# Kernel tuning notes

Measured on AMD Instinct MI355X. Metric: run time of the kernel, lower is better.

Reference implementation:

```python
import jax, jax.numpy as jnp
import numpy as np

N_NODES = 101001  # n_user + n_item + n_attr + 1
EMBED = 64
N_EDGES = 2020020  # ~avg degree 20
EPS = 1e-12


def setup_inputs() -> dict:
    key = jax.random.key(0)
    ks = jax.random.split(key, 8)
    h0 = jax.random.normal(ks[0], (N_NODES, EMBED), dtype=jnp.float32)
    h_att = jax.random.normal(ks[1], (N_NODES, EMBED), dtype=jnp.float32)
    t_att = jax.random.normal(ks[2], (N_NODES, EMBED), dtype=jnp.float32)
    w1 = jax.random.normal(ks[3], (EMBED, EMBED), dtype=jnp.float32) * (1.0 / np.sqrt(EMBED))
    b1 = jnp.zeros((EMBED,), dtype=jnp.float32)
    w2 = jax.random.normal(ks[4], (EMBED, EMBED), dtype=jnp.float32) * (1.0 / np.sqrt(EMBED))
    b2 = jnp.zeros((EMBED,), dtype=jnp.float32)
    edge_row = jnp.sort(jax.random.randint(ks[5], (N_EDGES,), 0, N_NODES, dtype=jnp.int32))
    edge_col = jax.random.randint(ks[6], (N_EDGES,), 0, N_NODES, dtype=jnp.int32)
    return {"h0": h0, "h_att": h_att, "t_att": t_att, "w1": w1, "b1": b1,
            "w2": w2, "b2": b2, "edge_row": edge_row, "edge_col": edge_col}


def _edge_softmax(h_att, t_att, edge_row, edge_col, n):
    # per-source-node softmax over ragged neighbor lists (kg_pair)
    logits = jnp.sum(h_att[edge_row] * t_att[edge_col], axis=-1)  # [E]
    m = jax.ops.segment_max(logits, edge_row, num_segments=n)
    e = jnp.exp(logits - m[edge_row])
    s = jax.ops.segment_sum(e, edge_row, num_segments=n)
    return e / jnp.maximum(s[edge_row], EPS)  # [E]


def reference(h0, h_att, t_att, w1, b1, w2, b2, edge_row, edge_col):
    n, d = h0.shape
    w = _edge_softmax(h_att, t_att, edge_row, edge_col, n)  # sparse attention weights
    h = h0
    all_embedding = [h0]
    for (W, b) in ((w1, b1), (w2, b2)):  # k = 1, 2 of ProP_n_Layer
        # n_embedding = SpMM(sp_weight, h)
        msg = jax.ops.segment_sum(w[:, None] * h[edge_col], edge_row, num_segments=n)
        add = h + msg
        h = jax.nn.relu(add @ W.T + b)
        norm = h / jnp.maximum(jnp.linalg.norm(h, axis=-1, keepdims=True), EPS)
        all_embedding.append(norm)
        h = norm  # normalized embedding feeds the next propagation layer
    return jnp.stack(all_embedding, axis=0)  # [n_layer, N, D]
```

## Files before the change

### kernel.cpp

```cpp
#include <hip/hip_runtime.h>
#include <math.h>

#define EMBED 64

__device__ __forceinline__ float dot4(float4 a, float4 b) {
    return fmaf(a.x, b.x, fmaf(a.y, b.y, fmaf(a.z, b.z, a.w * b.w)));
}

__device__ __forceinline__ float red16(float d) {
    d += __shfl_xor(d, 1);
    d += __shfl_xor(d, 2);
    d += __shfl_xor(d, 4);
    d += __shfl_xor(d, 8);
    return d;
}

__global__ void __launch_bounds__(256, 8) rowptr_logits_kernel(
        const float* __restrict__ ha, const float* __restrict__ ta,
        const int* __restrict__ row, const int* __restrict__ col,
        int* __restrict__ rp, float* __restrict__ logits,
        int E, int N, int totalThreads, int totalWaves) {
    int tid = blockIdx.x * blockDim.x + threadIdx.x;

    for (int i = tid; i < E; i += totalThreads) {
        if (i == 0) {
            int r0 = row[0];
            for (int r = 0; r <= r0; ++r) rp[r] = 0;
        } else {
            int a = row[i - 1], b = row[i];
            for (int r = a + 1; r <= b; ++r) rp[r] = i;
        }
        if (i == E - 1) {
            int rl = row[E - 1];
            for (int r = rl + 1; r <= N; ++r) rp[r] = E;
        }
    }

    int wid = tid >> 6;
    int lane = threadIdx.x & 63;
    int eg = lane >> 4, q = lane & 15;
    const float4* ha4 = (const float4*)ha;
    const float4* ta4 = (const float4*)ta;

    for (int base = wid * 16; base < E; base += totalWaves * 16) {
        int j0 = base + eg, j1 = base + 4 + eg, j2 = base + 8 + eg, j3 = base + 12 + eg;
        int i0 = min(j0, E - 1), i1 = min(j1, E - 1);
        int i2 = min(j2, E - 1), i3 = min(j3, E - 1);
        int r0 = row[i0], r1 = row[i1], r2 = row[i2], r3 = row[i3];
        int c0 = col[i0], c1 = col[i1], c2 = col[i2], c3 = col[i3];
        float4 t0 = ta4[(size_t)c0 * 16 + q];
        float4 t1 = ta4[(size_t)c1 * 16 + q];
        float4 t2 = ta4[(size_t)c2 * 16 + q];
        float4 t3 = ta4[(size_t)c3 * 16 + q];
        float4 a0 = ha4[(size_t)r0 * 16 + q];
        float4 a1 = ha4[(size_t)r1 * 16 + q];
        float4 a2 = ha4[(size_t)r2 * 16 + q];
        float4 a3 = ha4[(size_t)r3 * 16 + q];
        float d0 = red16(dot4(a0, t0));
        float d1 = red16(dot4(a1, t1));
        float d2 = red16(dot4(a2, t2));
        float d3 = red16(dot4(a3, t3));
        if (q == 0) {
            if (j0 < E) logits[j0] = d0;
            if (j1 < E) logits[j1] = d1;
            if (j2 < E) logits[j2] = d2;
            if (j3 < E) logits[j3] = d3;
        }
    }
}

__global__ void __launch_bounds__(256) copy_softmax_kernel(
        const float* __restrict__ h0, float* __restrict__ out0, int n4,
        const int* __restrict__ rp, float* __restrict__ lw, int N,
        int totalThreads, int totalWaves) {
    int tid = blockIdx.x * blockDim.x + threadIdx.x;
    for (int i = tid; i < n4; i += totalThreads)
        ((float4*)out0)[i] = ((const float4*)h0)[i];

    int wid = tid >> 6;
    int lane = threadIdx.x & 63;
    for (int n = wid; n < N; n += totalWaves) {
        int s = rp[n], t = rp[n + 1];
        int deg = t - s;
        if (deg <= 0) continue;
        if (deg <= 64) {
            float v = (lane < deg) ? lw[s + lane] : -1e30f;
            float m = v;
            #pragma unroll
            for (int off = 32; off > 0; off >>= 1) m = fmaxf(m, __shfl_xor(m, off));
            float e = (lane < deg) ? __expf(v - m) : 0.f;
            float sum = e;
            #pragma unroll
            for (int off = 32; off > 0; off >>= 1) sum += __shfl_xor(sum, off);
            float inv = 1.f / fmaxf(sum, 1e-12f);
            if (lane < deg) lw[s + lane] = e * inv;
        } else {
            float m = -1e30f;
            for (int e = s + lane; e < t; e += 64) m = fmaxf(m, lw[e]);
            #pragma unroll
            for (int off = 32; off > 0; off >>= 1) m = fmaxf(m, __shfl_xor(m, off));
            float sum = 0.f;
            for (int e = s + lane; e < t; e += 64) sum += __expf(lw[e] - m);
            #pragma unroll
            for (int off = 32; off > 0; off >>= 1) sum += __shfl_xor(sum, off);
            float inv = 1.f / fmaxf(sum, 1e-12f);
            for (int e = s + lane; e < t; e += 64) lw[e] = __expf(lw[e] - m) * inv;
        }
    }
}

__global__ void __launch_bounds__(256, 4) prop_layer_kernel(
        const float* __restrict__ h_in,
        const float* __restrict__ W, const float* __restrict__ b,
        const int* __restrict__ col, const float* __restrict__ ew,
        const int* __restrict__ rp,
        float* __restrict__ out, int N, int totalWaves) {
    __shared__ float4 rbuf[4][17];
    int wid = (blockIdx.x * blockDim.x + threadIdx.x) >> 6;
    int lane = threadIdx.x & 63;
    int ws = threadIdx.x >> 6;
    int eg = lane >> 4, q = lane & 15;
    const float4* h4 = (const float4*)h_in;

    float4 Wr[16];
    const float4* W4 = (const float4*)W;
    #pragma unroll
    for (int p = 0; p < 16; ++p) Wr[p] = W4[lane * 16 + p];
    float bias = b[lane];

    for (int n = wid; n < N; n += totalWaves) {
        int s = rp[n], t = rp[n + 1];
        float4 self = h4[(size_t)n * 16 + q];
        float4 a0 = make_float4(0.f, 0.f, 0.f, 0.f);
        float4 a1 = make_float4(0.f, 0.f, 0.f, 0.f);
        int e0 = s;
        for (; e0 + 16 <= t; e0 += 16) {
            int i0 = e0 + eg, i1 = e0 + 4 + eg, i2 = e0 + 8 + eg, i3 = e0 + 12 + eg;
            int c0 = col[i0], c1 = col[i1], c2 = col[i2], c3 = col[i3];
            float w0 = ew[i0], w1 = ew[i1], w2 = ew[i2], w3 = ew[i3];
            float4 v0 = h4[(size_t)c0 * 16 + q];
            float4 v1 = h4[(size_t)c1 * 16 + q];
            float4 v2 = h4[(size_t)c2 * 16 + q];
            float4 v3 = h4[(size_t)c3 * 16 + q];
            a0.x = fmaf(w0, v0.x, a0.x); a0.y = fmaf(w0, v0.y, a0.y);
            a0.z = fmaf(w0, v0.z, a0.z); a0.w = fmaf(w0, v0.w, a0.w);
            a1.x = fmaf(w1, v1.x, a1.x); a1.y = fmaf(w1, v1.y, a1.y);
            a1.z = fmaf(w1, v1.z, a1.z); a1.w = fmaf(w1, v1.w, a1.w);
            a0.x = fmaf(w2, v2.x, a0.x); a0.y = fmaf(w2, v2.y, a0.y);
            a0.z = fmaf(w2, v2.z, a0.z); a0.w = fmaf(w2, v2.w, a0.w);
            a1.x = fmaf(w3, v3.x, a1.x); a1.y = fmaf(w3, v3.y, a1.y);
            a1.z = fmaf(w3, v3.z, a1.z); a1.w = fmaf(w3, v3.w, a1.w);
        }
        if (e0 < t) {
            int j0 = e0 + eg, j1 = e0 + 4 + eg, j2 = e0 + 8 + eg, j3 = e0 + 12 + eg;
            int i0 = min(j0, t - 1), i1 = min(j1, t - 1);
            int i2 = min(j2, t - 1), i3 = min(j3, t - 1);
            int c0 = col[i0], c1 = col[i1], c2 = col[i2], c3 = col[i3];
            float w0 = (j0 < t) ? ew[i0] : 0.f;
            float w1 = (j1 < t) ? ew[i1] : 0.f;
            float w2 = (j2 < t) ? ew[i2] : 0.f;
            float w3 = (j3 < t) ? ew[i3] : 0.f;
            float4 v0 = h4[(size_t)c0 * 16 + q];
            float4 v1 = h4[(size_t)c1 * 16 + q];
            float4 v2 = h4[(size_t)c2 * 16 + q];
            float4 v3 = h4[(size_t)c3 * 16 + q];
            a0.x = fmaf(w0, v0.x, a0.x); a0.y = fmaf(w0, v0.y, a0.y);
            a0.z = fmaf(w0, v0.z, a0.z); a0.w = fmaf(w0, v0.w, a0.w);
            a1.x = fmaf(w1, v1.x, a1.x); a1.y = fmaf(w1, v1.y, a1.y);
            a1.z = fmaf(w1, v1.z, a1.z); a1.w = fmaf(w1, v1.w, a1.w);
            a0.x = fmaf(w2, v2.x, a0.x); a0.y = fmaf(w2, v2.y, a0.y);
            a0.z = fmaf(w2, v2.z, a0.z); a0.w = fmaf(w2, v2.w, a0.w);
            a1.x = fmaf(w3, v3.x, a1.x); a1.y = fmaf(w3, v3.y, a1.y);
            a1.z = fmaf(w3, v3.z, a1.z); a1.w = fmaf(w3, v3.w, a1.w);
        }
        a0.x += a1.x; a0.y += a1.y; a0.z += a1.z; a0.w += a1.w;
        a0.x += __shfl_xor(a0.x, 16); a0.y += __shfl_xor(a0.y, 16);
        a0.z += __shfl_xor(a0.z, 16); a0.w += __shfl_xor(a0.w, 16);
        a0.x += __shfl_xor(a0.x, 32); a0.y += __shfl_xor(a0.y, 32);
        a0.z += __shfl_xor(a0.z, 32); a0.w += __shfl_xor(a0.w, 32);

        if (eg == 0) {
            float4 r;
            r.x = self.x + a0.x; r.y = self.y + a0.y;
            r.z = self.z + a0.z; r.w = self.w + a0.w;
            rbuf[ws][q] = r;
        }
        asm volatile("s_waitcnt lgkmcnt(0)" ::: "memory");

        float x0 = bias, x1 = 0.f, x2 = 0.f, x3 = 0.f;
        #pragma unroll
        for (int j = 0; j < 4; ++j) {
            float4 b0 = rbuf[ws][4 * j + 0];
            float4 b1 = rbuf[ws][4 * j + 1];
            float4 b2 = rbuf[ws][4 * j + 2];
            float4 b3 = rbuf[ws][4 * j + 3];
            float4 w0 = Wr[4 * j + 0], w1 = Wr[4 * j + 1];
            float4 w2 = Wr[4 * j + 2], w3 = Wr[4 * j + 3];
            x0 = fmaf(b0.x, w0.x, x0); x0 = fmaf(b0.y, w0.y, x0);
            x0 = fmaf(b0.z, w0.z, x0); x0 = fmaf(b0.w, w0.w, x0);
            x1 = fmaf(b1.x, w1.x, x1); x1 = fmaf(b1.y, w1.y, x1);
            x1 = fmaf(b1.z, w1.z, x1); x1 = fmaf(b1.w, w1.w, x1);
            x2 = fmaf(b2.x, w2.x, x2); x2 = fmaf(b2.y, w2.y, x2);
            x2 = fmaf(b2.z, w2.z, x2); x2 = fmaf(b2.w, w2.w, x2);
            x3 = fmaf(b3.x, w3.x, x3); x3 = fmaf(b3.y, w3.y, x3);
            x3 = fmaf(b3.z, w3.z, x3); x3 = fmaf(b3.w, w3.w, x3);
        }
        float x = fmaxf((x0 + x1) + (x2 + x3), 0.f);

        float ss = x * x;
        #pragma unroll
        for (int off = 32; off > 0; off >>= 1) ss += __shfl_xor(ss, off);
        float scale = 1.f / fmaxf(sqrtf(ss), 1e-12f);
        out[(size_t)n * EMBED + lane] = x * scale;
    }
}

extern "C" void kernel_launch(void* const* d_in, const int* in_sizes, int n_in,
                              void* d_out, int out_size, void* d_ws, size_t ws_size,
                              hipStream_t stream) {
    const float* h0   = (const float*)d_in[0];
    const float* ha   = (const float*)d_in[1];
    const float* ta   = (const float*)d_in[2];
    const float* w1   = (const float*)d_in[3];
    const float* b1   = (const float*)d_in[4];
    const float* w2   = (const float*)d_in[5];
    const float* b2   = (const float*)d_in[6];
    const int*   erow = (const int*)d_in[7];
    const int*   ecol = (const int*)d_in[8];

    const int N = in_sizes[0] / EMBED;
    const int E = in_sizes[7];
    float* out = (float*)d_out;

    int*   rp = (int*)d_ws;
    size_t rp_bytes = ((size_t)(N + 1) * sizeof(int) + 255) & ~(size_t)255;
    float* ew = (float*)((char*)d_ws + rp_bytes);

    rowptr_logits_kernel<<<2048, 256, 0, stream>>>(
        ha, ta, erow, ecol, rp, ew, E, N, 2048 * 256, 2048 * 4);

    copy_softmax_kernel<<<2048, 256, 0, stream>>>(
        h0, out, N * EMBED / 4, rp, ew, N, 2048 * 256, 2048 * 4);

    float* out1 = out + (size_t)N * EMBED;
    float* out2 = out + 2 * (size_t)N * EMBED;
    prop_layer_kernel<<<1024, 256, 0, stream>>>(h0,   w1, b1, ecol, ew, rp, out1, N, 1024 * 4);
    prop_layer_kernel<<<1024, 256, 0, stream>>>(out1, w2, b2, ecol, ew, rp, out2, N, 1024 * 4);
}
```

Baseline: 416.7 us.

## Gather neighbor embeddings from half-precision shadow copies in SpMM layers

```diff
diff --git a/kernel.cpp b/kernel.cpp
--- a/kernel.cpp
+++ b/kernel.cpp
@@ -1,4 +1,5 @@
 #include <hip/hip_runtime.h>
+#include <hip/hip_fp16.h>
 #include <math.h>
 
 #define EMBED 64
@@ -13,6 +14,14 @@
     d += __shfl_xor(d, 4);
     d += __shfl_xor(d, 8);
     return d;
+}
+
+__device__ __forceinline__ void acc_h4(float4& A, float wt, float2 g) {
+    const __half2* p = (const __half2*)&g;
+    float2 lo = __half22float2(p[0]);
+    float2 hi = __half22float2(p[1]);
+    A.x = fmaf(wt, lo.x, A.x); A.y = fmaf(wt, lo.y, A.y);
+    A.z = fmaf(wt, hi.x, A.z); A.w = fmaf(wt, hi.y, A.w);
 }
 
 __global__ void __launch_bounds__(256, 8) rowptr_logits_kernel(
@@ -71,11 +80,22 @@
 
 __global__ void __launch_bounds__(256) copy_softmax_kernel(
         const float* __restrict__ h0, float* __restrict__ out0, int n4,
+        float2* __restrict__ hh0,
         const int* __restrict__ rp, float* __restrict__ lw, int N,
         int totalThreads, int totalWaves) {
     int tid = blockIdx.x * blockDim.x + threadIdx.x;
-    for (int i = tid; i < n4; i += totalThreads)
-        ((float4*)out0)[i] = ((const float4*)h0)[i];
+    for (int i = tid; i < n4; i += totalThreads) {
+        float4 v = ((const float4*)h0)[i];
+        ((float4*)out0)[i] = v;
+        if (hh0) {
+            __half2 a = __floats2half2_rn(v.x, v.y);
+            __half2 b = __floats2half2_rn(v.z, v.w);
+            float2 pk;
+            *(__half2*)&pk.x = a;
+            *(__half2*)&pk.y = b;
+            hh0[i] = pk;
+        }
+    }
 
     int wid = tid >> 6;
     int lane = threadIdx.x & 63;
@@ -109,6 +129,125 @@
     }
 }
 
+__global__ void __launch_bounds__(256, 4) prop_layer_f16_kernel(
+        const float* __restrict__ h_in,
+        const float2* __restrict__ hh_in,
+        const float* __restrict__ W, const float* __restrict__ b,
+        const int* __restrict__ col, const float* __restrict__ ew,
+        const int* __restrict__ rp,
+        float* __restrict__ out, __half* __restrict__ hh_out,
+        int N, int totalWaves) {
+    __shared__ float4 rbuf[4][17];
+    int wid = (blockIdx.x * blockDim.x + threadIdx.x) >> 6;
+    int lane = threadIdx.x & 63;
+    int ws = threadIdx.x >> 6;
+    int eg = lane >> 4, q = lane & 15;
+    const float4* h4 = (const float4*)h_in;
+
+    float4 Wr[16];
+    const float4* W4 = (const float4*)W;
+    #pragma unroll
+    for (int p = 0; p < 16; ++p) Wr[p] = W4[lane * 16 + p];
+    float bias = b[lane];
+
+    for (int n = wid; n < N; n += totalWaves) {
+        int s = rp[n], t = rp[n + 1];
+        float4 self = h4[(size_t)n * 16 + q];
+        float4 a0 = make_float4(0.f, 0.f, 0.f, 0.f);
+        float4 a1 = make_float4(0.f, 0.f, 0.f, 0.f);
+        int e0 = s;
+        for (; e0 + 32 <= t; e0 += 32) {
+            int i0 = e0 + eg,      i1 = e0 + 4 + eg,  i2 = e0 + 8 + eg,  i3 = e0 + 12 + eg;
+            int i4 = e0 + 16 + eg, i5 = e0 + 20 + eg, i6 = e0 + 24 + eg, i7 = e0 + 28 + eg;
+            int c0 = col[i0], c1 = col[i1], c2 = col[i2], c3 = col[i3];
+            int c4 = col[i4], c5 = col[i5], c6 = col[i6], c7 = col[i7];
+            float w0 = ew[i0], w1 = ew[i1], w2 = ew[i2], w3 = ew[i3];
+            float w4 = ew[i4], w5 = ew[i5], w6 = ew[i6], w7 = ew[i7];
+            float2 g0 = hh_in[(size_t)c0 * 16 + q];
+            float2 g1 = hh_in[(size_t)c1 * 16 + q];
+            float2 g2 = hh_in[(size_t)c2 * 16 + q];
+            float2 g3 = hh_in[(size_t)c3 * 16 + q];
+            float2 g4 = hh_in[(size_t)c4 * 16 + q];
+            float2 g5 = hh_in[(size_t)c5 * 16 + q];
+            float2 g6 = hh_in[(size_t)c6 * 16 + q];
+            float2 g7 = hh_in[(size_t)c7 * 16 + q];
+            acc_h4(a0, w0, g0); acc_h4(a1, w1, g1);
+            acc_h4(a0, w2, g2); acc_h4(a1, w3, g3);
+            acc_h4(a0, w4, g4); acc_h4(a1, w5, g5);
+            acc_h4(a0, w6, g6); acc_h4(a1, w7, g7);
+        }
+        if (e0 < t) {
+            int j0 = e0 + eg,      j1 = e0 + 4 + eg,  j2 = e0 + 8 + eg,  j3 = e0 + 12 + eg;
+            int j4 = e0 + 16 + eg, j5 = e0 + 20 + eg, j6 = e0 + 24 + eg, j7 = e0 + 28 + eg;
+            int i0 = min(j0, t - 1), i1 = min(j1, t - 1), i2 = min(j2, t - 1), i3 = min(j3, t - 1);
+            int i4 = min(j4, t - 1), i5 = min(j5, t - 1), i6 = min(j6, t - 1), i7 = min(j7, t - 1);
+            int c0 = col[i0], c1 = col[i1], c2 = col[i2], c3 = col[i3];
+            int c4 = col[i4], c5 = col[i5], c6 = col[i6], c7 = col[i7];
+            float w0 = (j0 < t) ? ew[i0] : 0.f;
+            float w1 = (j1 < t) ? ew[i1] : 0.f;
+            float w2 = (j2 < t) ? ew[i2] : 0.f;
+            float w3 = (j3 < t) ? ew[i3] : 0.f;
+            float w4 = (j4 < t) ? ew[i4] : 0.f;
+            float w5 = (j5 < t) ? ew[i5] : 0.f;
+            float w6 = (j6 < t) ? ew[i6] : 0.f;
+            float w7 = (j7 < t) ? ew[i7] : 0.f;
+            float2 g0 = hh_in[(size_t)c0 * 16 + q];
+            float2 g1 = hh_in[(size_t)c1 * 16 + q];
+            float2 g2 = hh_in[(size_t)c2 * 16 + q];
+            float2 g3 = hh_in[(size_t)c3 * 16 + q];
+            float2 g4 = hh_in[(size_t)c4 * 16 + q];
+            float2 g5 = hh_in[(size_t)c5 * 16 + q];
+            float2 g6 = hh_in[(size_t)c6 * 16 + q];
+            float2 g7 = hh_in[(size_t)c7 * 16 + q];
+            acc_h4(a0, w0, g0); acc_h4(a1, w1, g1);
+            acc_h4(a0, w2, g2); acc_h4(a1, w3, g3);
+            acc_h4(a0, w4, g4); acc_h4(a1, w5, g5);
+            acc_h4(a0, w6, g6); acc_h4(a1, w7, g7);
+        }
+        a0.x += a1.x; a0.y += a1.y; a0.z += a1.z; a0.w += a1.w;
+        a0.x += __shfl_xor(a0.x, 16); a0.y += __shfl_xor(a0.y, 16);
+        a0.z += __shfl_xor(a0.z, 16); a0.w += __shfl_xor(a0.w, 16);
+        a0.x += __shfl_xor(a0.x, 32); a0.y += __shfl_xor(a0.y, 32);
+        a0.z += __shfl_xor(a0.z, 32); a0.w += __shfl_xor(a0.w, 32);
+
+        if (eg == 0) {
+            float4 r;
+            r.x = self.x + a0.x; r.y = self.y + a0.y;
+            r.z = self.z + a0.z; r.w = self.w + a0.w;
+            rbuf[ws][q] = r;
+        }
+        asm volatile("s_waitcnt lgkmcnt(0)" ::: "memory");
+
+        float x0 = bias, x1 = 0.f, x2 = 0.f, x3 = 0.f;
+        #pragma unroll
+        for (int j = 0; j < 4; ++j) {
+            float4 b0 = rbuf[ws][4 * j + 0];
+            float4 b1 = rbuf[ws][4 * j + 1];
+            float4 b2 = rbuf[ws][4 * j + 2];
+            float4 b3 = rbuf[ws][4 * j + 3];
+            float4 w0 = Wr[4 * j + 0], w1 = Wr[4 * j + 1];
+            float4 w2 = Wr[4 * j + 2], w3 = Wr[4 * j + 3];
+            x0 = fmaf(b0.x, w0.x, x0); x0 = fmaf(b0.y, w0.y, x0);
+            x0 = fmaf(b0.z, w0.z, x0); x0 = fmaf(b0.w, w0.w, x0);
+            x1 = fmaf(b1.x, w1.x, x1); x1 = fmaf(b1.y, w1.y, x1);
+            x1 = fmaf(b1.z, w1.z, x1); x1 = fmaf(b1.w, w1.w, x1);
+            x2 = fmaf(b2.x, w2.x, x2); x2 = fmaf(b2.y, w2.y, x2);
+            x2 = fmaf(b2.z, w2.z, x2); x2 = fmaf(b2.w, w2.w, x2);
+            x3 = fmaf(b3.x, w3.x, x3); x3 = fmaf(b3.y, w3.y, x3);
+            x3 = fmaf(b3.z, w3.z, x3); x3 = fmaf(b3.w, w3.w, x3);
+        }
+        float x = fmaxf((x0 + x1) + (x2 + x3), 0.f);
+
+        float ss = x * x;
+        #pragma unroll
+        for (int off = 32; off > 0; off >>= 1) ss += __shfl_xor(ss, off);
+        float scale = 1.f / fmaxf(sqrtf(ss), 1e-12f);
+        float xs = x * scale;
+        out[(size_t)n * EMBED + lane] = xs;
+        if (hh_out) hh_out[(size_t)n * EMBED + lane] = __float2half(xs);
+    }
+}
+
 __global__ void __launch_bounds__(256, 4) prop_layer_kernel(
         const float* __restrict__ h_in,
         const float* __restrict__ W, const float* __restrict__ b,
@@ -232,18 +371,32 @@
     const int E = in_sizes[7];
     float* out = (float*)d_out;
 
-    int*   rp = (int*)d_ws;
-    size_t rp_bytes = ((size_t)(N + 1) * sizeof(int) + 255) & ~(size_t)255;
-    float* ew = (float*)((char*)d_ws + rp_bytes);
+    size_t rpB = ((size_t)(N + 1) * sizeof(int) + 255) & ~(size_t)255;
+    size_t ewB = ((size_t)E * sizeof(float) + 255) & ~(size_t)255;
+    size_t hB  = ((size_t)N * EMBED * sizeof(__half) + 255) & ~(size_t)255;
+    bool use_f16 = (ws_size >= rpB + ewB + 2 * hB);
+
+    int*    rp  = (int*)d_ws;
+    float*  ew  = (float*)((char*)d_ws + rpB);
+    __half* hh0 = (__half*)((char*)d_ws + rpB + ewB);
+    __half* hh1 = (__half*)((char*)d_ws + rpB + ewB + hB);
 
     rowptr_logits_kernel<<<2048, 256, 0, stream>>>(
         ha, ta, erow, ecol, rp, ew, E, N, 2048 * 256, 2048 * 4);
 
     copy_softmax_kernel<<<2048, 256, 0, stream>>>(
-        h0, out, N * EMBED / 4, rp, ew, N, 2048 * 256, 2048 * 4);
+        h0, out, N * EMBED / 4, use_f16 ? (float2*)hh0 : nullptr,
+        rp, ew, N, 2048 * 256, 2048 * 4);
 
     float* out1 = out + (size_t)N * EMBED;
     float* out2 = out + 2 * (size_t)N * EMBED;
-    prop_layer_kernel<<<1024, 256, 0, stream>>>(h0,   w1, b1, ecol, ew, rp, out1, N, 1024 * 4);
-    prop_layer_kernel<<<1024, 256, 0, stream>>>(out1, w2, b2, ecol, ew, rp, out2, N, 1024 * 4);
-}
+    if (use_f16) {
+        prop_layer_f16_kernel<<<1024, 256, 0, stream>>>(
+            h0, (const float2*)hh0, w1, b1, ecol, ew, rp, out1, hh1, N, 1024 * 4);
+        prop_layer_f16_kernel<<<1024, 256, 0, stream>>>(
+            out1, (const float2*)hh1, w2, b2, ecol, ew, rp, out2, nullptr, N, 1024 * 4);
+    } else {
+        prop_layer_kernel<<<1024, 256, 0, stream>>>(h0,   w1, b1, ecol, ew, rp, out1, N, 1024 * 4);
+        prop_layer_kernel<<<1024, 256, 0, stream>>>(out1, w2, b2, ecol, ew, rp, out2, N, 1024 * 4);
+    }
+}
```

Result: no change. 424.8 us (+2.0%).
